# Kernel tuning notes

Measured on AMD Instinct MI355X. Metric: run time of the kernel, lower is better.

## Reference

```python
import jax, jax.numpy as jnp
from jax import lax
import numpy as np

B, CIN, COUT, H, W = 8, 64, 64, 128, 128
K = 3
KK = K * K  # 9 kernel taps


def setup_inputs() -> dict:
    key = jax.random.key(0)
    ks = jax.random.split(key, 10)
    n = jax.random.normal
    s = 0.05  # keep activations in a sane range
    return {
        "Fi": n(ks[0], (B, CIN, H, W), jnp.float32),
        "Fe": n(ks[1], (B, CIN, H, W), jnp.float32),
        "w1": n(ks[2], (CIN, 2 * CIN, 5, 5), jnp.float32) * s,
        "b1": n(ks[3], (CIN,), jnp.float32) * s,
        "w2": n(ks[4], (CIN, CIN, 3, 3), jnp.float32) * s,
        "b2": n(ks[5], (CIN,), jnp.float32) * s,
        "w_off": n(ks[6], (3 * KK, CIN, 3, 3), jnp.float32) * s,
        "b_off": n(ks[7], (3 * KK,), jnp.float32) * s,
        "w_dcn": n(ks[8], (COUT, CIN, 3, 3), jnp.float32) * s,
        "b_dcn": n(ks[9], (COUT,), jnp.float32) * s,
    }


def _conv(x, w, b, pad):
    y = lax.conv_general_dilated(x, w, (1, 1), [(pad, pad), (pad, pad)],
                                 dimension_numbers=('NCHW', 'OIHW', 'NCHW'))
    return y + b[None, :, None, None]


def _leaky(x):
    return jnp.where(x >= 0, x, 0.1 * x)  # LeakyReLU(0.1)


def _bilinear(img, y, x):
    # img [B,C,H,W]; y, x [B,KK,H,W] fractional sampling coords; zero padding OOB
    Bn, C, Hi, Wi = img.shape
    y0 = jnp.floor(y)
    x0 = jnp.floor(x)
    flat = img.reshape(Bn, C, Hi * Wi)
    out = jnp.zeros((Bn, C) + y.shape[1:], img.dtype)
    for dy, dx in ((0, 0), (0, 1), (1, 0), (1, 1)):
        yi = y0 + dy
        xi = x0 + dx
        wgt = (1.0 - jnp.abs(y - yi)) * (1.0 - jnp.abs(x - xi))
        valid = (yi >= 0) & (yi <= Hi - 1) & (xi >= 0) & (xi <= Wi - 1)
        yc = jnp.clip(yi, 0, Hi - 1).astype(jnp.int32)
        xc = jnp.clip(xi, 0, Wi - 1).astype(jnp.int32)
        idx = (yc * Wi + xc).reshape(Bn, 1, -1)
        v = jnp.take_along_axis(flat, jnp.broadcast_to(idx, (Bn, C, idx.shape[-1])), axis=2)
        v = v.reshape(Bn, C, *y.shape[1:])  # [B,C,KK,H,W]
        out = out + v * (wgt * valid)[:, None]
    return out


def _dcn(x, feat, w_off, b_off, w, b):
    # modulated deformable conv (DCNv2), k=3, stride=1, pad=1, dilation=1
    oo = _conv(feat, w_off, b_off, 1)                 # [B, 3*KK, H, W]
    o1, o2, m = jnp.split(oo, 3, axis=1)              # dy, dx, mask logits
    offset_out = jnp.concatenate([o1, o2], axis=1)
    mask = jax.nn.sigmoid(m)                          # [B,KK,H,W]
    ky, kx = jnp.meshgrid(jnp.arange(K), jnp.arange(K), indexing='ij')
    ky = ky.reshape(KK)
    kx = kx.reshape(KK)
    base_y = (jnp.arange(H)[None, :, None] - 1 + ky[:, None, None]).astype(x.dtype)  # [KK,H,1]
    base_x = (jnp.arange(W)[None, None, :] - 1 + kx[:, None, None]).astype(x.dtype)  # [KK,1,W]
    ys = base_y[None] + o1                            # [B,KK,H,W]
    xs = base_x[None] + o2                            # [B,KK,H,W]
    samp = _bilinear(x, ys, xs) * mask[:, None]       # [B,C,KK,H,W]
    out = jnp.einsum('bckhw,ock->bohw', samp, w.reshape(w.shape[0], w.shape[1], KK))
    return offset_out, out + b[None, :, None, None]


def reference(Fi, Fe, w1, b1, w2, b2, w_off, b_off, w_dcn, b_dcn):
    feat = _leaky(_conv(jnp.concatenate([Fi, Fe], axis=1), w1, b1, 2))
    feat = _leaky(_conv(feat, w2, b2, 1))
    offset_out, aligned = _dcn(Fe, feat, w_off, b_off, w_dcn, b_dcn)
    Ff = jnp.concatenate([Fi, aligned], axis=1)
    return offset_out, Ff
```

## Files before the change

kernel.cpp:

```cpp
#include <hip/hip_runtime.h>
#include <hip/hip_bf16.h>

typedef __bf16 bf16_t;
typedef __attribute__((ext_vector_type(8))) __bf16 bf16x8;
typedef __attribute__((ext_vector_type(4))) float f32x4;

#define Bn 8
#define Hh 128
#define Ww 128
#define HW 16384

#define WP1_B   ((size_t)0)
#define WP2_B   ((size_t)409600)
#define WPO_B   ((size_t)483328)
#define WDCN_B  ((size_t)520192)
#define BIAS_B  ((size_t)667648)
#define XT_B    ((size_t)668672)
#define F1_B    (XT_B + 33554432)
#define F2_B    (F1_B + 16777216)

__global__ void prep_kernel(const float* __restrict__ w1, const float* __restrict__ w2,
                            const float* __restrict__ woff, const float* __restrict__ wdcn,
                            const float* __restrict__ b1, const float* __restrict__ b2,
                            const float* __restrict__ boff, const float* __restrict__ bdcn,
                            char* __restrict__ wsb) {
    bf16_t* wp1 = (bf16_t*)(wsb + WP1_B);
    bf16_t* wp2 = (bf16_t*)(wsb + WP2_B);
    bf16_t* wpo = (bf16_t*)(wsb + WPO_B);
    bf16_t* wd  = (bf16_t*)(wsb + WDCN_B);
    float*  bias= (float*)(wsb + BIAS_B);
    int tid = blockIdx.x * blockDim.x + threadIdx.x;
    int nt  = gridDim.x * blockDim.x;
    for (int i = tid; i < 25*4*4*64*8; i += nt) {
        int j = i & 7, q = i >> 3;
        int n = q % 64; q /= 64;
        int g = q & 3;  q >>= 2;
        int ck = q & 3; int t = q >> 2;
        int cin = ck*32 + g*8 + j;
        wp1[i] = (bf16_t)w1[(n*128 + cin)*25 + t];
    }
    for (int i = tid; i < 9*2*4*64*8; i += nt) {
        int j = i & 7, q = i >> 3;
        int n = q % 64; q /= 64;
        int g = q & 3;  q >>= 2;
        int ck = q & 1; int t = q >> 1;
        int cin = ck*32 + g*8 + j;
        wp2[i] = (bf16_t)w2[(n*64 + cin)*9 + t];
    }
    for (int i = tid; i < 9*2*4*32*8; i += nt) {
        int j = i & 7, q = i >> 3;
        int n = q & 31; q >>= 5;
        int g = q & 3;  q >>= 2;
        int ck = q & 1; int t = q >> 1;
        int cin = ck*32 + g*8 + j;
        wpo[i] = (n < 27) ? (bf16_t)woff[(n*64 + cin)*9 + t] : (bf16_t)0.f;
    }
    for (int i = tid; i < 18*4*4*16*8; i += nt) {
        int j = i & 7, f = i >> 3;
        int l15 = f & 15; f >>= 4;
        int l4  = f & 3;  f >>= 2;
        int ntl = f & 3;  int kc = f >> 2;
        int kg = kc*32 + l4*8 + j;
        int tap = kg >> 6, c = kg & 63;
        int n = ntl*16 + l15;
        wd[i] = (bf16_t)wdcn[n*576 + c*9 + tap];
    }
    if (tid < 64) { bias[tid] = b1[tid]; bias[64+tid] = b2[tid]; bias[160+tid] = bdcn[tid]; }
    if (tid >= 64 && tid < 96) { int n = tid - 64; bias[128+n] = (n < 27) ? boff[n] : 0.f; }
}

__global__ __launch_bounds__(256) void nhwc_kernel(const float* __restrict__ Fi,
                                                   const float* __restrict__ Fe,
                                                   bf16_t* __restrict__ Xt) {
    __shared__ bf16_t tile[64][136];
    const int b  = blockIdx.y;
    const int p0 = blockIdx.x * 64;
    const int px = threadIdx.x & 63;
    const int csub = threadIdx.x >> 6;
    for (int ci = 0; ci < 32; ++ci) {
        int c = csub * 32 + ci;
        const float* src = (c < 64) ? (Fi + (((size_t)(b*64 + c)) << 14))
                                    : (Fe + (((size_t)(b*64 + (c-64))) << 14));
        tile[px][c] = (bf16_t)src[p0 + px];
    }
    __syncthreads();
    const int px2 = threadIdx.x >> 2;
    const int cc  = (threadIdx.x & 3) * 32;
    bf16x8* dst = (bf16x8*)(Xt + ((size_t)(b*HW) + p0 + px2) * 128 + cc);
    const bf16x8* srcl = (const bf16x8*)(&tile[px2][cc]);
    dst[0] = srcl[0]; dst[1] = srcl[1]; dst[2] = srcl[2]; dst[3] = srcl[3];
}

template <int CIN_, int KS, int COUTP, bool LEAKY, bool OUTF32, bool OFFS>
__global__ __launch_bounds__(256) void conv_mfma(const bf16_t* __restrict__ Xt,
                                                 const bf16_t* __restrict__ Wp,
                                                 const float* __restrict__ bias,
                                                 bf16_t* __restrict__ outb,
                                                 float* __restrict__ outf,
                                                 float* __restrict__ out0) {
    constexpr int PAD = KS / 2;
    constexpr int HR  = 4 + KS - 1;
    constexpr int HC  = 64 + KS - 1;
    constexpr int NC  = CIN_ / 32;
    constexpr int NT  = COUTP / 16;
    __shared__ bf16_t stg[HR * HC * 40];

    const int tid  = threadIdx.x;
    const int lane = tid & 63;
    const int wid  = tid >> 6;
    const int b    = blockIdx.z;
    const int h0   = blockIdx.y * 4;
    const int w0   = blockIdx.x * 64;
    const int l15  = lane & 15;
    const int l4   = lane >> 4;

    f32x4 acc[4][NT];
#pragma unroll
    for (int m = 0; m < 4; ++m)
#pragma unroll
        for (int nt = 0; nt < NT; ++nt)
#pragma unroll
            for (int r = 0; r < 4; ++r) acc[m][nt][r] = 0.f;

    const bf16_t Z0 = (bf16_t)0.f;
    const bf16x8 zv = {Z0, Z0, Z0, Z0, Z0, Z0, Z0, Z0};
    const bf16x8* wpt = (const bf16x8*)Wp;

    for (int ck = 0; ck < NC; ++ck) {
        for (int s = tid; s < HR * HC; s += 256) {
            const int srow = s / HC, scol = s % HC;
            const int gh = h0 - PAD + srow, gw = w0 - PAD + scol;
            bf16x8 v0 = zv, v1 = zv, v2 = zv, v3 = zv;
            if (((unsigned)gh < 128u) && ((unsigned)gw < 128u)) {
                const bf16x8* gp = (const bf16x8*)(Xt + (((size_t)(b*HW) + (gh << 7) + gw)) * CIN_ + ck * 32);
                v0 = gp[0]; v1 = gp[1]; v2 = gp[2]; v3 = gp[3];
            }
            bf16x8* ldst = (bf16x8*)(&stg[s * 40]);
            ldst[0] = v0; ldst[1] = v1; ldst[2] = v2; ldst[3] = v3;
        }
        __syncthreads();
        int t = 0;
#pragma unroll
        for (int dy = 0; dy < KS; ++dy) {
#pragma unroll
            for (int dx = 0; dx < KS; ++dx, ++t) {
                bf16x8 a[4];
#pragma unroll
                for (int m = 0; m < 4; ++m)
                    a[m] = *(const bf16x8*)(&stg[((wid + dy) * HC + (m * 16 + l15 + dx)) * 40 + l4 * 8]);
                bf16x8 bb[NT];
#pragma unroll
                for (int nt = 0; nt < NT; ++nt)
                    bb[nt] = wpt[((size_t)((t * NC + ck) * 4 + l4)) * COUTP + nt * 16 + l15];
#pragma unroll
                for (int m = 0; m < 4; ++m)
#pragma unroll
                    for (int nt = 0; nt < NT; ++nt)
                        acc[m][nt] = __builtin_amdgcn_mfma_f32_16x16x32_bf16(a[m], bb[nt], acc[m][nt], 0, 0, 0);
            }
        }
        __syncthreads();
    }

    const int hrow = h0 + wid;
#pragma unroll
    for (int m = 0; m < 4; ++m) {
#pragma unroll
        for (int nt = 0; nt < NT; ++nt) {
            const int n = nt * 16 + l15;
            const float bs = bias[n];
#pragma unroll
            for (int r = 0; r < 4; ++r) {
                const int px = w0 + m * 16 + l4 * 4 + r;
                float v = acc[m][nt][r] + bs;
                if (LEAKY) v = (v >= 0.f) ? v : 0.1f * v;
                const size_t pix = (size_t)(hrow << 7) + px;
                if (OUTF32) outf[(((size_t)(b * COUTP + n)) << 14) + pix] = v;
                else        outb[(((size_t)(b * HW)) + pix) * COUTP + n] = (bf16_t)v;
                if (OFFS) {
                    if (n < 18) out0[(((size_t)(b * 18 + n)) << 14) + pix] = v;
                }
            }
        }
    }
}

__global__ void copy_fi(const float* __restrict__ Fi, float* __restrict__ out1) {
    const int b = blockIdx.y;
    const int i = blockIdx.x * blockDim.x + threadIdx.x;
    const int e = i << 2;
    const int c = e >> 14;
    const int p = e & 16383;
    const float4* src = reinterpret_cast<const float4*>(Fi);
    float4* dst = reinterpret_cast<float4*>(out1);
    size_t se = ((size_t)b << 20) + e;
    size_t de = (((size_t)(b * 128 + c)) << 14) + p;
    dst[de >> 2] = src[se >> 2];
}

__global__ __launch_bounds__(256, 4) void dcn_mfma(const bf16_t* __restrict__ Xt,
                                                   const float* __restrict__ OO,
                                                   const bf16_t* __restrict__ Wd,
                                                   const float* __restrict__ bias,
                                                   float* __restrict__ out1) {
    const int tid  = threadIdx.x;
    const int lane = tid & 63;
    const int wave = tid >> 6;
    const int l15  = lane & 15;
    const int l4   = lane >> 4;
    const int blk  = blockIdx.x;
    const int b    = blk & 7;
    const int p0   = (blk >> 3) * 64 + wave * 16;

    f32x4 acc[4];
#pragma unroll
    for (int nt = 0; nt < 4; ++nt) {
        const float bs = bias[nt * 16 + l15];
        acc[nt][0] = bs; acc[nt][1] = bs; acc[nt][2] = bs; acc[nt][3] = bs;
    }

    const bf16_t* feb = Xt + ((size_t)(b * HW)) * 128 + 64;
    const bf16x8* Wdv = (const bf16x8*)Wd;

    const int p = p0 + l15;
    const int h = p >> 7, w = p & 127;
    const size_t oobase = (((size_t)(b * 32)) << 14) + p;
    const int c0 = l4 * 8;
    const int c1 = 32 + l4 * 8;

    float ys[9], xs[9], ms[9];
#pragma unroll
    for (int k = 0; k < 9; ++k) {
        const float o1v = OO[oobase + ((size_t)k << 14)];
        const float o2v = OO[oobase + ((size_t)(9 + k) << 14)];
        const float mlv = OO[oobase + ((size_t)(18 + k) << 14)];
        ys[k] = (float)(h - 1 + (k / 3)) + o1v;
        xs[k] = (float)(w - 1 + (k % 3)) + o2v;
        ms[k] = 1.f / (1.f + __expf(-mlv));
    }

    bf16x8 g[2][4];
    float  wq[2][4];
    int    toff[4];

#define DCN_ISSUE_EVEN(k)                                                        \
    do {                                                                         \
        const float yk = ys[(k)], xk = xs[(k)];                                  \
        const float y0f = floorf(yk), x0f = floorf(xk);                          \
        const float fy = yk - y0f, fx = xk - x0f;                                \
        const int y0 = (int)y0f, x0 = (int)x0f;                                  \
        const bool vy0 = (unsigned)y0 < 128u;                                    \
        const bool vy1 = (unsigned)(y0 + 1) < 128u;                              \
        const bool vx0 = (unsigned)x0 < 128u;                                    \
        const bool vx1 = (unsigned)(x0 + 1) < 128u;                              \
        const int y0c = min(max(y0, 0), 127), y1c = min(max(y0 + 1, 0), 127);    \
        const int x0c = min(max(x0, 0), 127), x1c = min(max(x0 + 1, 0), 127);    \
        const float mk = ms[(k)];                                                \
        float a00 = (1.f - fy) * (1.f - fx) * mk; a00 = (vy0 && vx0) ? a00 : 0.f;\
        float a01 = (1.f - fy) * fx * mk;         a01 = (vy0 && vx1) ? a01 : 0.f;\
        float a10 = fy * (1.f - fx) * mk;         a10 = (vy1 && vx0) ? a10 : 0.f;\
        float a11 = fy * fx * mk;                 a11 = (vy1 && vx1) ? a11 : 0.f;\
        wq[0][0] = a00; wq[0][1] = a01; wq[0][2] = a10; wq[0][3] = a11;          \
        toff[0] = (y0c << 7) + x0c; toff[1] = (y0c << 7) + x1c;                  \
        toff[2] = (y1c << 7) + x0c; toff[3] = (y1c << 7) + x1c;                  \
        g[0][0] = *(const bf16x8*)(feb + (((size_t)toff[0]) << 7) + c0);         \
        g[0][1] = *(const bf16x8*)(feb + (((size_t)toff[1]) << 7) + c0);         \
        g[0][2] = *(const bf16x8*)(feb + (((size_t)toff[2]) << 7) + c0);         \
        g[0][3] = *(const bf16x8*)(feb + (((size_t)toff[3]) << 7) + c0);         \
    } while (0)

#define DCN_ISSUE_ODD()                                                          \
    do {                                                                         \
        wq[1][0] = wq[0][0]; wq[1][1] = wq[0][1];                                \
        wq[1][2] = wq[0][2]; wq[1][3] = wq[0][3];                                \
        g[1][0] = *(const bf16x8*)(feb + (((size_t)toff[0]) << 7) + c1);         \
        g[1][1] = *(const bf16x8*)(feb + (((size_t)toff[1]) << 7) + c1);         \
        g[1][2] = *(const bf16x8*)(feb + (((size_t)toff[2]) << 7) + c1);         \
        g[1][3] = *(const bf16x8*)(feb + (((size_t)toff[3]) << 7) + c1);         \
    } while (0)

#define DCN_CONSUME(s)                                                           \
    do {                                                                         \
        bf16x8 af;                                                               \
        _Pragma("unroll")                                                        \
        for (int j = 0; j < 8; ++j)                                              \
            af[j] = (bf16_t)(wq[(s) & 1][0] * (float)g[(s) & 1][0][j]            \
                           + wq[(s) & 1][1] * (float)g[(s) & 1][1][j]            \
                           + wq[(s) & 1][2] * (float)g[(s) & 1][2][j]            \
                           + wq[(s) & 1][3] * (float)g[(s) & 1][3][j]);          \
        _Pragma("unroll")                                                        \
        for (int nt = 0; nt < 4; ++nt) {                                         \
            const bf16x8 bfr = Wdv[(((s) * 4 + nt) * 4 + l4) * 16 + l15];        \
            acc[nt] = __builtin_amdgcn_mfma_f32_16x16x32_bf16(af, bfr, acc[nt], 0, 0, 0); \
        }                                                                        \
    } while (0)

    DCN_ISSUE_EVEN(0);
#pragma unroll
    for (int s = 0; s < 18; ++s) {
        if (s + 1 < 18) {
            if ((s + 1) & 1) DCN_ISSUE_ODD();
            else             DCN_ISSUE_EVEN((s + 1) >> 1);
        }
        DCN_CONSUME(s);
    }

#undef DCN_ISSUE_EVEN
#undef DCN_ISSUE_ODD
#undef DCN_CONSUME

#pragma unroll
    for (int nt = 0; nt < 4; ++nt) {
        const int o = nt * 16 + l15;
#pragma unroll
        for (int r = 0; r < 4; ++r) {
            const int px = p0 + l4 * 4 + r;
            out1[(((size_t)(b * 128 + 64 + o)) << 14) + px] = acc[nt][r];
        }
    }
}

extern "C" void kernel_launch(void* const* d_in, const int* in_sizes, int n_in,
                              void* d_out, int out_size, void* d_ws, size_t ws_size,
                              hipStream_t stream) {
    const float* Fi    = (const float*)d_in[0];
    const float* Fe    = (const float*)d_in[1];
    const float* w1    = (const float*)d_in[2];
    const float* b1    = (const float*)d_in[3];
    const float* w2    = (const float*)d_in[4];
    const float* b2    = (const float*)d_in[5];
    const float* w_off = (const float*)d_in[6];
    const float* b_off = (const float*)d_in[7];
    const float* w_dcn = (const float*)d_in[8];
    const float* b_dcn = (const float*)d_in[9];

    char* wsb = (char*)d_ws;
    bf16_t* wp1   = (bf16_t*)(wsb + WP1_B);
    bf16_t* wp2   = (bf16_t*)(wsb + WP2_B);
    bf16_t* wpo   = (bf16_t*)(wsb + WPO_B);
    bf16_t* wdcnf = (bf16_t*)(wsb + WDCN_B);
    float*  bias  = (float*)(wsb + BIAS_B);
    bf16_t* Xt    = (bf16_t*)(wsb + XT_B);
    bf16_t* feat1 = (bf16_t*)(wsb + F1_B);
    bf16_t* feat2 = (bf16_t*)(wsb + F2_B);
    float*  OO    = (float*)(wsb + F1_B);

    float* out0 = (float*)d_out;
    float* out1 = out0 + (size_t)Bn * 18 * HW;

    prep_kernel<<<256, 256, 0, stream>>>(w1, w2, w_off, w_dcn, b1, b2, b_off, b_dcn, wsb);

    nhwc_kernel<<<dim3(256, 8), 256, 0, stream>>>(Fi, Fe, Xt);

    conv_mfma<128, 5, 64, true, false, false>
        <<<dim3(2, 32, 8), 256, 0, stream>>>(Xt, wp1, bias, feat1, nullptr, nullptr);

    conv_mfma<64, 3, 64, true, false, false>
        <<<dim3(2, 32, 8), 256, 0, stream>>>(feat1, wp2, bias + 64, feat2, nullptr, nullptr);

    conv_mfma<64, 3, 32, false, true, true>
        <<<dim3(2, 32, 8), 256, 0, stream>>>(feat2, wpo, bias + 128, nullptr, OO, out0);

    copy_fi<<<dim3(1024, 8), 256, 0, stream>>>(Fi, out1);

    dcn_mfma<<<2048, 256, 0, stream>>>(Xt, OO, wdcnf, bias + 160, out1);
}
```

Before: 334.3 us.

## Fuse Fi copy into NHWC transpose and deepen DCN gather prefetch pipeline

The separate copy_fi kernel is removed, and the NHWC transpose kernel now writes Fi straight into the output while it reads it, saving one launch and one re-read of Fi. The DCN kernel's gather pipeline grows from double to quadruple buffering, issuing loads three steps ahead so more gather latency is hidden behind MFMA work. Register demand rises, so the launch bounds occupancy hint drops from 4 to 3 blocks per CU, trading occupancy for memory-level parallelism within each thread.

```diff
diff --git a/kernel.cpp b/kernel.cpp
--- a/kernel.cpp
+++ b/kernel.cpp
@@ -71,7 +71,8 @@
 
 __global__ __launch_bounds__(256) void nhwc_kernel(const float* __restrict__ Fi,
                                                    const float* __restrict__ Fe,
-                                                   bf16_t* __restrict__ Xt) {
+                                                   bf16_t* __restrict__ Xt,
+                                                   float* __restrict__ out1) {
     __shared__ bf16_t tile[64][136];
     const int b  = blockIdx.y;
     const int p0 = blockIdx.x * 64;
@@ -81,7 +82,9 @@
         int c = csub * 32 + ci;
         const float* src = (c < 64) ? (Fi + (((size_t)(b*64 + c)) << 14))
                                     : (Fe + (((size_t)(b*64 + (c-64))) << 14));
-        tile[px][c] = (bf16_t)src[p0 + px];
+        const float v = src[p0 + px];
+        tile[px][c] = (bf16_t)v;
+        if (c < 64) out1[(((size_t)(b*128 + c)) << 14) + p0 + px] = v;
     }
     __syncthreads();
     const int px2 = threadIdx.x >> 2;
@@ -185,20 +188,7 @@
     }
 }
 
-__global__ void copy_fi(const float* __restrict__ Fi, float* __restrict__ out1) {
-    const int b = blockIdx.y;
-    const int i = blockIdx.x * blockDim.x + threadIdx.x;
-    const int e = i << 2;
-    const int c = e >> 14;
-    const int p = e & 16383;
-    const float4* src = reinterpret_cast<const float4*>(Fi);
-    float4* dst = reinterpret_cast<float4*>(out1);
-    size_t se = ((size_t)b << 20) + e;
-    size_t de = (((size_t)(b * 128 + c)) << 14) + p;
-    dst[de >> 2] = src[se >> 2];
-}
-
-__global__ __launch_bounds__(256, 4) void dcn_mfma(const bf16_t* __restrict__ Xt,
+__global__ __launch_bounds__(256, 3) void dcn_mfma(const bf16_t* __restrict__ Xt,
                                                    const float* __restrict__ OO,
                                                    const bf16_t* __restrict__ Wd,
                                                    const float* __restrict__ bias,
@@ -239,13 +229,14 @@
         ms[k] = 1.f / (1.f + __expf(-mlv));
     }
 
-    bf16x8 g[2][4];
-    float  wq[2][4];
+    bf16x8 g[4][4];
+    float  wq[4][4];
     int    toff[4];
 
-#define DCN_ISSUE_EVEN(k)                                                        \
+#define DCN_ISSUE_E(s)                                                           \
     do {                                                                         \
-        const float yk = ys[(k)], xk = xs[(k)];                                  \
+        const int k_ = (s) >> 1, sl_ = (s) & 3;                                  \
+        const float yk = ys[k_], xk = xs[k_];                                    \
         const float y0f = floorf(yk), x0f = floorf(xk);                          \
         const float fy = yk - y0f, fx = xk - x0f;                                \
         const int y0 = (int)y0f, x0 = (int)x0f;                                  \
@@ -255,39 +246,41 @@
         const bool vx1 = (unsigned)(x0 + 1) < 128u;                              \
         const int y0c = min(max(y0, 0), 127), y1c = min(max(y0 + 1, 0), 127);    \
         const int x0c = min(max(x0, 0), 127), x1c = min(max(x0 + 1, 0), 127);    \
-        const float mk = ms[(k)];                                                \
+        const float mk = ms[k_];                                                 \
         float a00 = (1.f - fy) * (1.f - fx) * mk; a00 = (vy0 && vx0) ? a00 : 0.f;\
         float a01 = (1.f - fy) * fx * mk;         a01 = (vy0 && vx1) ? a01 : 0.f;\
         float a10 = fy * (1.f - fx) * mk;         a10 = (vy1 && vx0) ? a10 : 0.f;\
         float a11 = fy * fx * mk;                 a11 = (vy1 && vx1) ? a11 : 0.f;\
-        wq[0][0] = a00; wq[0][1] = a01; wq[0][2] = a10; wq[0][3] = a11;          \
+        wq[sl_][0] = a00; wq[sl_][1] = a01; wq[sl_][2] = a10; wq[sl_][3] = a11;  \
         toff[0] = (y0c << 7) + x0c; toff[1] = (y0c << 7) + x1c;                  \
         toff[2] = (y1c << 7) + x0c; toff[3] = (y1c << 7) + x1c;                  \
-        g[0][0] = *(const bf16x8*)(feb + (((size_t)toff[0]) << 7) + c0);         \
-        g[0][1] = *(const bf16x8*)(feb + (((size_t)toff[1]) << 7) + c0);         \
-        g[0][2] = *(const bf16x8*)(feb + (((size_t)toff[2]) << 7) + c0);         \
-        g[0][3] = *(const bf16x8*)(feb + (((size_t)toff[3]) << 7) + c0);         \
+        g[sl_][0] = *(const bf16x8*)(feb + (((size_t)toff[0]) << 7) + c0);       \
+        g[sl_][1] = *(const bf16x8*)(feb + (((size_t)toff[1]) << 7) + c0);       \
+        g[sl_][2] = *(const bf16x8*)(feb + (((size_t)toff[2]) << 7) + c0);       \
+        g[sl_][3] = *(const bf16x8*)(feb + (((size_t)toff[3]) << 7) + c0);       \
     } while (0)
 
-#define DCN_ISSUE_ODD()                                                          \
+#define DCN_ISSUE_O(s)                                                           \
     do {                                                                         \
-        wq[1][0] = wq[0][0]; wq[1][1] = wq[0][1];                                \
-        wq[1][2] = wq[0][2]; wq[1][3] = wq[0][3];                                \
-        g[1][0] = *(const bf16x8*)(feb + (((size_t)toff[0]) << 7) + c1);         \
-        g[1][1] = *(const bf16x8*)(feb + (((size_t)toff[1]) << 7) + c1);         \
-        g[1][2] = *(const bf16x8*)(feb + (((size_t)toff[2]) << 7) + c1);         \
-        g[1][3] = *(const bf16x8*)(feb + (((size_t)toff[3]) << 7) + c1);         \
+        const int sl_ = (s) & 3, pe_ = ((s) - 1) & 3;                            \
+        wq[sl_][0] = wq[pe_][0]; wq[sl_][1] = wq[pe_][1];                        \
+        wq[sl_][2] = wq[pe_][2]; wq[sl_][3] = wq[pe_][3];                        \
+        g[sl_][0] = *(const bf16x8*)(feb + (((size_t)toff[0]) << 7) + c1);       \
+        g[sl_][1] = *(const bf16x8*)(feb + (((size_t)toff[1]) << 7) + c1);       \
+        g[sl_][2] = *(const bf16x8*)(feb + (((size_t)toff[2]) << 7) + c1);       \
+        g[sl_][3] = *(const bf16x8*)(feb + (((size_t)toff[3]) << 7) + c1);       \
     } while (0)
 
 #define DCN_CONSUME(s)                                                           \
     do {                                                                         \
+        const int sl_ = (s) & 3;                                                 \
         bf16x8 af;                                                               \
         _Pragma("unroll")                                                        \
         for (int j = 0; j < 8; ++j)                                              \
-            af[j] = (bf16_t)(wq[(s) & 1][0] * (float)g[(s) & 1][0][j]            \
-                           + wq[(s) & 1][1] * (float)g[(s) & 1][1][j]            \
-                           + wq[(s) & 1][2] * (float)g[(s) & 1][2][j]            \
-                           + wq[(s) & 1][3] * (float)g[(s) & 1][3][j]);          \
+            af[j] = (bf16_t)(wq[sl_][0] * (float)g[sl_][0][j]                    \
+                           + wq[sl_][1] * (float)g[sl_][1][j]                    \
+                           + wq[sl_][2] * (float)g[sl_][2][j]                    \
+                           + wq[sl_][3] * (float)g[sl_][3][j]);                  \
         _Pragma("unroll")                                                        \
         for (int nt = 0; nt < 4; ++nt) {                                         \
             const bf16x8 bfr = Wdv[(((s) * 4 + nt) * 4 + l4) * 16 + l15];        \
@@ -295,18 +288,20 @@
         }                                                                        \
     } while (0)
 
-    DCN_ISSUE_EVEN(0);
+    DCN_ISSUE_E(0);
+    DCN_ISSUE_O(1);
+    DCN_ISSUE_E(2);
 #pragma unroll
     for (int s = 0; s < 18; ++s) {
-        if (s + 1 < 18) {
-            if ((s + 1) & 1) DCN_ISSUE_ODD();
-            else             DCN_ISSUE_EVEN((s + 1) >> 1);
+        if (s + 3 < 18) {
+            if ((s + 3) & 1) DCN_ISSUE_O(s + 3);
+            else             DCN_ISSUE_E(s + 3);
         }
         DCN_CONSUME(s);
     }
 
-#undef DCN_ISSUE_EVEN
-#undef DCN_ISSUE_ODD
+#undef DCN_ISSUE_E
+#undef DCN_ISSUE_O
 #undef DCN_CONSUME
 
 #pragma unroll
@@ -350,7 +345,7 @@
 
     prep_kernel<<<256, 256, 0, stream>>>(w1, w2, w_off, w_dcn, b1, b2, b_off, b_dcn, wsb);
 
-    nhwc_kernel<<<dim3(256, 8), 256, 0, stream>>>(Fi, Fe, Xt);
+    nhwc_kernel<<<dim3(256, 8), 256, 0, stream>>>(Fi, Fe, Xt, out1);
 
     conv_mfma<128, 5, 64, true, false, false>
         <<<dim3(2, 32, 8), 256, 0, stream>>>(Xt, wp1, bias, feat1, nullptr, nullptr);
@@ -361,7 +356,5 @@
     conv_mfma<64, 3, 32, false, true, true>
         <<<dim3(2, 32, 8), 256, 0, stream>>>(feat2, wpo, bias + 128, nullptr, OO, out0);
 
-    copy_fi<<<dim3(1024, 8), 256, 0, stream>>>(Fi, out1);
-
     dcn_mfma<<<2048, 256, 0, stream>>>(Xt, OO, wdcnf, bias + 160, out1);
 }
```

After: 335.6 us. Within noise of the previous version (+0.4%).
